# Kernel optimization log

Hardware: AMD Instinct MI355X
Metric: run time of the kernel (lower is better)

The kernel has to match this reference:

```python
import jax, jax.numpy as jnp
import numpy as np

B, S, D, H = 8, 1024, 1024, 16
DH = D // H  # 64

def setup_inputs() -> dict:
    key = jax.random.key(0)
    k1, k2, k3 = jax.random.split(key, 3)
    x = jax.random.normal(k1, (B, S, D), dtype=jnp.float32)
    mask = jnp.tril(jnp.ones((S, S), dtype=bool))[None, None]  # causal [1,1,S,S]
    W_qkv = jax.random.normal(k2, (D, 3 * D), dtype=jnp.float32) * 0.02
    W_out = jax.random.normal(k3, (D, D), dtype=jnp.float32) * 0.02
    return {"x": x, "mask": mask, "W_qkv": W_qkv, "W_out": W_out}

def reference(x, mask, W_qkv, W_out):
    qkv = jnp.einsum('bnd,de->bne', x, W_qkv)
    q, k, v = jnp.split(qkv, 3, axis=-1)
    # [b, h, n, dh]
    split_heads = lambda t: t.reshape(B, S, H, DH).transpose(0, 2, 1, 3)
    q, k, v = map(split_heads, (q, k, v))
    attn = jnp.einsum('bhnd,bhmd->bhnm', q, k) / jnp.sqrt(jnp.float32(DH))
    attn = jnp.where(mask, attn, 0.7 * jnp.finfo(attn.dtype).min)
    attn = jax.nn.softmax(attn.astype(jnp.float32), axis=-1).astype(x.dtype)
    out = jnp.einsum('bhnm,bhmd->bhnd', attn, v)
    out = out.transpose(0, 2, 1, 3).reshape(B, S, D)
    return jnp.einsum('bnd,de->bne', out, W_out)
```

## Files before the change

### kernel.cpp

```cpp
#include <hip/hip_runtime.h>
#include <stdint.h>

typedef __attribute__((ext_vector_type(8))) short short8;
typedef __attribute__((ext_vector_type(4))) float floatx4;

__device__ __forceinline__ unsigned short f2bf(float f) {
  union { float f; uint32_t u; } v; v.f = f;
  uint32_t u = v.u;
  return (unsigned short)((u + 0x7FFFu + ((u >> 16) & 1u)) >> 16);
}

__device__ __forceinline__ uint32_t fbits(float f) {
  union { float f; uint32_t u; } v; v.f = f; return v.u;
}
__device__ __forceinline__ uint32_t pkbf(float hi, float lo) {
  return __builtin_amdgcn_perm(fbits(hi), fbits(lo), 0x07060302u);
}

__device__ __forceinline__ void gl_lds16(const void* g, void* l) {
  __builtin_amdgcn_global_load_lds((__attribute__((address_space(1))) void*)g,
                                   (__attribute__((address_space(3))) void*)l,
                                   16, 0, 0);
}

__global__ __launch_bounds__(256) void prep_kernel(const float* __restrict__ x,
                                                   unsigned short* __restrict__ xb,
                                                   const float* __restrict__ Wqkv,
                                                   unsigned short* __restrict__ WqkvT,
                                                   const float* __restrict__ Wout,
                                                   unsigned short* __restrict__ WoutT) {
  __shared__ float tile[32][33];
  int id = blockIdx.x;
  if (id < 8192) {
    int i = id * 256 + threadIdx.x;
    float4 v = ((const float4*)x)[i];
    ushort4 o;
    o.x = f2bf(v.x); o.y = f2bf(v.y); o.z = f2bf(v.z); o.w = f2bf(v.w);
    ((ushort4*)xb)[i] = o;
    return;
  }
  id -= 8192;
  int bx = id & 127, r0 = (id >> 7) * 32;
  const int R = 1024;
  const float* in; unsigned short* out; int C;
  if (bx < 96) { in = Wqkv; out = WqkvT; C = 3072; }
  else         { in = Wout; out = WoutT; C = 1024; bx -= 96; }
  int c0 = bx * 32;
  int tx = threadIdx.x & 31;
  int ty = threadIdx.x >> 5;
  for (int i = ty; i < 32; i += 8)
    tile[i][tx] = in[(size_t)(r0 + i) * C + c0 + tx];
  __syncthreads();
  for (int i = ty; i < 32; i += 8)
    out[(size_t)(c0 + i) * R + r0 + tx] = f2bf(tile[tx][i]);
}

__global__ __launch_bounds__(256) void gemm_bt_kernel(const unsigned short* __restrict__ A,
                                                      const unsigned short* __restrict__ Bt,
                                                      int N, int mode,
                                                      unsigned short* __restrict__ qo,
                                                      unsigned short* __restrict__ ko,
                                                      unsigned short* __restrict__ vo,
                                                      float* __restrict__ fo) {
  const int Kd = 1024;
  __shared__ union {
    struct { unsigned short A[2][8192]; unsigned short B[2][8192]; } s;
    float cf[16384];
    unsigned short ch[32768];
  } sm;
  const int tid = threadIdx.x;
  const int w = tid >> 6, lane = tid & 63;
  const int quad = lane >> 4, l16 = lane & 15;
  const int l7 = l16 & 7;
  const int wm = w >> 1, wn = w & 1;
  const int m0 = blockIdx.y * 128, n0 = blockIdx.x * 128;
  const int tr = (mode == 0) && (n0 >= 2048);
  const int r8 = lane >> 3, ch = lane & 7;
  const int sw = (ch ^ r8) * 8;

  floatx4 acc[4][4];
#pragma unroll
  for (int i = 0; i < 4; ++i)
#pragma unroll
    for (int j = 0; j < 4; ++j)
      acc[i][j] = (floatx4){0.f, 0.f, 0.f, 0.f};

  auto stage = [&](int it, int buf) {
    const int k0 = it * 64;
#pragma unroll
    for (int i = 0; i < 4; ++i) {
      const int row = i * 32 + w * 8 + r8;
      gl_lds16(A + (size_t)(m0 + row) * Kd + k0 + sw, (char*)&sm.s.A[buf][0] + i * 4096 + w * 1024);
      gl_lds16(Bt + (size_t)(n0 + row) * Kd + k0 + sw, (char*)&sm.s.B[buf][0] + i * 4096 + w * 1024);
    }
  };

  stage(0, 0);
  __syncthreads();

  for (int it = 0; it < 16; ++it) {
    const int buf = it & 1;
    if (it < 15) stage(it + 1, buf ^ 1);
    const char* Ab = (const char*)&sm.s.A[buf][0];
    const char* Bb = (const char*)&sm.s.B[buf][0];
#pragma unroll
    for (int half = 0; half < 2; ++half) {
      short8 af[4], bf[4];
#pragma unroll
      for (int i = 0; i < 4; ++i)
        af[i] = *(const short8*)(Ab + (wm * 64 + i * 16 + l16) * 128 +
                                 (((half << 2) | quad) ^ l7) * 16);
#pragma unroll
      for (int j = 0; j < 4; ++j)
        bf[j] = *(const short8*)(Bb + (wn * 64 + j * 16 + l16) * 128 +
                                 (((half << 2) | quad) ^ l7) * 16);
      if (!tr) {
#pragma unroll
        for (int i = 0; i < 4; ++i)
#pragma unroll
          for (int j = 0; j < 4; ++j)
            acc[i][j] = __builtin_amdgcn_mfma_f32_16x16x32_bf16(af[i], bf[j], acc[i][j], 0, 0, 0);
      } else {
#pragma unroll
        for (int p = 0; p < 4; ++p)
#pragma unroll
          for (int q = 0; q < 4; ++q)
            acc[p][q] = __builtin_amdgcn_mfma_f32_16x16x32_bf16(bf[p], af[q], acc[p][q], 0, 0, 0);
      }
    }
    __syncthreads();
  }

  if (mode == 1) {
    float* Cs = sm.cf;
#pragma unroll
    for (int i = 0; i < 4; ++i)
#pragma unroll
      for (int j = 0; j < 4; ++j)
#pragma unroll
        for (int r = 0; r < 4; ++r) {
          int row = wm * 64 + i * 16 + quad * 4 + r;
          int col = wn * 64 + j * 16 + l16;
          Cs[row * 128 + (col ^ ((row & 7) << 2))] = acc[i][j][r];
        }
    __syncthreads();
#pragma unroll
    for (int c = 0; c < 16; ++c) {
      int idx = c * 256 + tid;
      int row = idx >> 5, fc = idx & 31;
      float4 v = *(const float4*)&sm.cf[row * 128 + ((fc ^ (row & 7)) << 2)];
      *(float4*)&fo[(size_t)(m0 + row) * N + n0 + fc * 4] = v;
    }
  } else {
    unsigned short* Cs = sm.ch;
    if (!tr) {
#pragma unroll
      for (int i = 0; i < 4; ++i)
#pragma unroll
        for (int j = 0; j < 4; ++j)
#pragma unroll
          for (int r = 0; r < 4; ++r) {
            int row = wm * 64 + i * 16 + quad * 4 + r;
            int col = wn * 64 + j * 16 + l16;
            Cs[row * 128 + (col ^ ((row & 7) << 3))] = f2bf(acc[i][j][r]);
          }
    } else {
#pragma unroll
      for (int p = 0; p < 4; ++p)
#pragma unroll
        for (int q = 0; q < 4; ++q)
#pragma unroll
          for (int r = 0; r < 4; ++r) {
            int row = wn * 64 + p * 16 + quad * 4 + r;
            int col = wm * 64 + q * 16 + l16;
            Cs[row * 128 + (col ^ ((row & 7) << 3))] = f2bf(acc[p][q][r]);
          }
    }
    __syncthreads();
    unsigned short* dst0 = (n0 < 1024) ? qo : ko;
#pragma unroll
    for (int c = 0; c < 8; ++c) {
      int idx = c * 256 + tid;
      int row = idx >> 4, lc = idx & 15;
      short8 v = *(const short8*)&sm.ch[row * 128 + ((lc ^ (row & 7)) << 3)];
      int col = lc * 8;
      if (!tr) {
        int m = m0 + row, n = n0 + col;
        int h = (n & 1023) >> 6, dh = n & 63;
        int bb = m >> 10, s = m & 1023;
        *(short8*)&dst0[(size_t)(bb * 16 + h) * 65536 + (size_t)s * 64 + dh] = v;
      } else {
        int n = n0 + row, m = m0 + col;
        int h = (n & 1023) >> 6, dh = n & 63;
        int bb = m >> 10, s0 = m & 1023;
        *(short8*)&vo[(size_t)(bb * 16 + h) * 65536 + (size_t)dh * 1024 + s0] = v;
      }
    }
  }
}

__global__ __launch_bounds__(512, 2) void gemm_qkv_kernel(const unsigned short* __restrict__ A,
                                                          const unsigned short* __restrict__ Bt,
                                                          unsigned short* __restrict__ qo,
                                                          unsigned short* __restrict__ ko,
                                                          unsigned short* __restrict__ vo) {
  __shared__ union {
    struct { unsigned short A[2][16384]; unsigned short B[2][8192]; } s;
    unsigned short ch[49152];
  } sm;
  const int tid = threadIdx.x;
  const int w = tid >> 6, lane = tid & 63;
  const int quad = lane >> 4, l16 = lane & 15, l7 = l16 & 7;
  const int wm = w >> 1, wn = w & 1;
  const int m0 = blockIdx.y * 256, n0 = blockIdx.x * 128;
  const bool tr = (n0 >= 2048);
  const int r8 = lane >> 3, ch8 = lane & 7;
  const int sw = (ch8 ^ r8) * 8;

  floatx4 acc[16];
#pragma unroll
  for (int i = 0; i < 16; ++i) acc[i] = (floatx4){0.f, 0.f, 0.f, 0.f};

  auto stageA = [&](int t, int buf) {
    const int k0 = t * 64;
#pragma unroll
    for (int i = 0; i < 4; ++i) {
      const int row = i * 64 + w * 8 + r8;
      gl_lds16(A + (size_t)(m0 + row) * 1024 + k0 + sw,
               (char*)&sm.s.A[buf][0] + (i * 64 + w * 8) * 128);
    }
  };
  auto stageB = [&](int t, int buf) {
    const int k0 = t * 64;
#pragma unroll
    for (int i = 0; i < 2; ++i) {
      const int row = i * 64 + w * 8 + r8;
      gl_lds16(Bt + (size_t)(n0 + row) * 1024 + k0 + sw,
               (char*)&sm.s.B[buf][0] + (i * 64 + w * 8) * 128);
    }
  };

  stageA(0, 0); stageB(0, 0);
  stageA(1, 1); stageB(1, 1);
  asm volatile("s_waitcnt vmcnt(6)" ::: "memory");
  __builtin_amdgcn_s_barrier();

  const int cK0 = (quad ^ l7) * 16;
  const int cK1 = ((4 | quad) ^ l7) * 16;
  const int arow = (wm * 64 + l16) * 128;
  const int brow = (wn * 64 + l16) * 128;

  short8 af[2][2];
  short8 bf[2][2][2];

#define MFMA8(MH, NH)                                                              \
  do {                                                                             \
    if (!tr) {                                                                     \
      _Pragma("unroll") for (int kk = 0; kk < 2; ++kk)                             \
      _Pragma("unroll") for (int m = 0; m < 2; ++m)                                \
      _Pragma("unroll") for (int n = 0; n < 2; ++n)                                \
        acc[((MH)*2 + m) * 4 + (NH)*2 + n] = __builtin_amdgcn_mfma_f32_16x16x32_bf16( \
            af[m][kk], bf[NH][n][kk], acc[((MH)*2 + m) * 4 + (NH)*2 + n], 0, 0, 0);   \
    } else {                                                                       \
      _Pragma("unroll") for (int kk = 0; kk < 2; ++kk)                             \
      _Pragma("unroll") for (int n = 0; n < 2; ++n)                                \
      _Pragma("unroll") for (int m = 0; m < 2; ++m)                                \
        acc[((NH)*2 + n) * 4 + (MH)*2 + m] = __builtin_amdgcn_mfma_f32_16x16x32_bf16( \
            bf[NH][n][kk], af[m][kk], acc[((NH)*2 + n) * 4 + (MH)*2 + m], 0, 0, 0);   \
    }                                                                              \
  } while (0)

  for (int t = 0; t < 16; ++t) {
    const int buf = t & 1;
    const char* Ab = (const char*)&sm.s.A[buf][0];
    const char* Bb = (const char*)&sm.s.B[buf][0];

#pragma unroll
    for (int m = 0; m < 2; ++m) {
      af[m][0] = *(const short8*)(Ab + arow + m * 2048 + cK0);
      af[m][1] = *(const short8*)(Ab + arow + m * 2048 + cK1);
    }
#pragma unroll
    for (int n = 0; n < 2; ++n) {
      bf[0][n][0] = *(const short8*)(Bb + brow + n * 2048 + cK0);
      bf[0][n][1] = *(const short8*)(Bb + brow + n * 2048 + cK1);
    }
    __builtin_amdgcn_s_barrier();
    asm volatile("s_waitcnt lgkmcnt(0)" ::: "memory");
    __builtin_amdgcn_s_setprio(1);
    MFMA8(0, 0);
    __builtin_amdgcn_s_setprio(0);
    __builtin_amdgcn_sched_barrier(0);
    __builtin_amdgcn_s_barrier();

#pragma unroll
    for (int n = 0; n < 2; ++n) {
      bf[1][n][0] = *(const short8*)(Bb + brow + (2 + n) * 2048 + cK0);
      bf[1][n][1] = *(const short8*)(Bb + brow + (2 + n) * 2048 + cK1);
    }
    __builtin_amdgcn_s_barrier();
    asm volatile("s_waitcnt lgkmcnt(0)" ::: "memory");
    __builtin_amdgcn_s_setprio(1);
    MFMA8(0, 1);
    __builtin_amdgcn_s_setprio(0);
    __builtin_amdgcn_sched_barrier(0);
    __builtin_amdgcn_s_barrier();

#pragma unroll
    for (int m = 0; m < 2; ++m) {
      af[m][0] = *(const short8*)(Ab + arow + (2 + m) * 2048 + cK0);
      af[m][1] = *(const short8*)(Ab + arow + (2 + m) * 2048 + cK1);
    }
    if (t < 14) stageB(t + 2, buf);
    __builtin_amdgcn_s_barrier();
    asm volatile("s_waitcnt lgkmcnt(0)" ::: "memory");
    __builtin_amdgcn_s_setprio(1);
    MFMA8(1, 1);
    __builtin_amdgcn_s_setprio(0);
    __builtin_amdgcn_sched_barrier(0);
    __builtin_amdgcn_s_barrier();

    if (t < 14) {
      stageA(t + 2, buf);
      asm volatile("s_waitcnt vmcnt(6)" ::: "memory");
    } else {
      asm volatile("s_waitcnt vmcnt(0)" ::: "memory");
    }
    __builtin_amdgcn_s_barrier();
    __builtin_amdgcn_s_setprio(1);
    MFMA8(1, 0);
    __builtin_amdgcn_s_setprio(0);
    __builtin_amdgcn_sched_barrier(0);
    __builtin_amdgcn_s_barrier();
  }
#undef MFMA8

  unsigned short* Cs = sm.ch;
  if (!tr) {
#pragma unroll
    for (int mf = 0; mf < 4; ++mf)
#pragma unroll
      for (int nf = 0; nf < 4; ++nf)
#pragma unroll
        for (int r = 0; r < 4; ++r) {
          int row = wm * 64 + mf * 16 + quad * 4 + r;
          int col = wn * 64 + nf * 16 + l16;
          Cs[row * 128 + (col ^ ((row & 7) << 3))] = f2bf(acc[mf * 4 + nf][r]);
        }
    __syncthreads();
    unsigned short* dst0 = (n0 < 1024) ? qo : ko;
#pragma unroll
    for (int c = 0; c < 8; ++c) {
      int idx = c * 512 + tid;
      int row = idx >> 4, lc = idx & 15;
      short8 v = *(const short8*)&Cs[row * 128 + ((lc ^ (row & 7)) << 3)];
      int m = m0 + row, n = n0 + lc * 8;
      int h = (n & 1023) >> 6, dh = n & 63;
      int bb = m >> 10, s = m & 1023;
      *(short8*)&dst0[(size_t)(bb * 16 + h) * 65536 + (size_t)s * 64 + dh] = v;
    }
  } else {
#pragma unroll
    for (int nf = 0; nf < 4; ++nf)
#pragma unroll
      for (int mf = 0; mf < 4; ++mf)
#pragma unroll
        for (int r = 0; r < 4; ++r) {
          int row = wn * 64 + nf * 16 + quad * 4 + r;
          int col = wm * 64 + mf * 16 + l16;
          Cs[row * 256 + (col ^ ((row & 7) << 3))] = f2bf(acc[nf * 4 + mf][r]);
        }
    __syncthreads();
#pragma unroll
    for (int c = 0; c < 8; ++c) {
      int idx = c * 512 + tid;
      int row = idx >> 5, lc = idx & 31;
      short8 v = *(const short8*)&Cs[row * 256 + ((lc ^ (row & 7)) << 3)];
      int n = n0 + row, m = m0 + lc * 8;
      int h = (n & 1023) >> 6, dh = n & 63;
      int bb = m >> 10, s = m & 1023;
      *(short8*)&vo[(size_t)(bb * 16 + h) * 65536 + (size_t)dh * 1024 + s] = v;
    }
  }
}

__global__ __launch_bounds__(256, 2) void attn_kernel(const unsigned short* __restrict__ Qb,
                                                      const unsigned short* __restrict__ Kb,
                                                      const unsigned short* __restrict__ VbT,
                                                      unsigned short* __restrict__ AOb) {
  __shared__ unsigned short Kt[2][4096];
  __shared__ unsigned short Vt[2][4096];
  const int tid = threadIdx.x;
  const int w = tid >> 6, lane = tid & 63;
  const int quad = lane >> 4, l16 = lane & 15;
  const int l7 = l16 & 7;
  const int id = blockIdx.x;
  const int by = id >> 2;
  const int p = id & 3;
  const int bb = by >> 4, hh = by & 15;
  const int qlo = p * 128 + w * 32;
  const int qhi = (7 - p) * 128 + w * 32;
  const unsigned short* Qp = Qb + (size_t)by * 65536;
  const unsigned short* Kp = Kb + (size_t)by * 65536;
  const unsigned short* Vp = VbT + (size_t)by * 65536;

  short8 bq[2][2][2];
#pragma unroll
  for (int g = 0; g < 2; ++g)
#pragma unroll
    for (int qt = 0; qt < 2; ++qt)
#pragma unroll
      for (int kh = 0; kh < 2; ++kh)
        bq[g][qt][kh] = *(const short8*)(Qp + (size_t)((g ? qhi : qlo) + qt * 16 + l16) * 64 +
                                         kh * 32 + quad * 8);

  floatx4 o[2][2][4];
  floatx4 ps[2][2];
#pragma unroll
  for (int g = 0; g < 2; ++g)
#pragma unroll
    for (int qt = 0; qt < 2; ++qt) {
      ps[g][qt] = (floatx4){0.f, 0.f, 0.f, 0.f};
#pragma unroll
      for (int dt = 0; dt < 4; ++dt) o[g][qt][dt] = (floatx4){0.f, 0.f, 0.f, 0.f};
    }

  short8 ones;
#pragma unroll
  for (int i = 0; i < 8; ++i) ones[i] = (short)0x3F80;

  const int T = 16 - 2 * p;
  const int r8 = lane >> 3, ch = lane & 7;
  const int sw8 = (ch ^ r8) * 8;

  auto stage = [&](int t, int buf) {
    const int n0 = t * 64;
#pragma unroll
    for (int i = 0; i < 2; ++i) {
      const int c = w * 2 + i;
      const int row = c * 8 + r8;
      gl_lds16(Kp + (size_t)(n0 + row) * 64 + sw8, (char*)&Kt[buf][0] + c * 1024);
      gl_lds16(Vp + (size_t)row * 1024 + n0 + sw8, (char*)&Vt[buf][0] + c * 1024);
    }
  };

  stage(0, 0);
  __syncthreads();

  for (int t = 0; t < T; ++t) {
    const int buf = t & 1;
    if (t + 1 < T) stage(t + 1, buf ^ 1);
    const int n0 = t * 64;
    const bool alo = (n0 <= qlo + 31), ahi = (n0 <= qhi + 31);
    if (alo | ahi) {
      const char* kbase = (const char*)&Kt[buf][0];
      const char* vbase = (const char*)&Vt[buf][0];
      short8 ak[4][2];
#pragma unroll
      for (int kt = 0; kt < 4; ++kt)
#pragma unroll
        for (int kh = 0; kh < 2; ++kh)
          ak[kt][kh] = *(const short8*)(kbase + (kt * 16 + l16) * 128 +
                                        (((kh << 2) | quad) ^ l7) * 16);
      union PaU { short8 v; uint32_t d[4]; };
      PaU pa[2][2][2];

      auto score = [&](int g, int qb) {
        const bool full = (n0 + 63 <= qb);
#pragma unroll
        for (int kt = 0; kt < 4; ++kt)
#pragma unroll
          for (int qt = 0; qt < 2; ++qt) {
            floatx4 s = (floatx4){0.f, 0.f, 0.f, 0.f};
            s = __builtin_amdgcn_mfma_f32_16x16x32_bf16(ak[kt][0], bq[g][qt][0], s, 0, 0, 0);
            s = __builtin_amdgcn_mfma_f32_16x16x32_bf16(ak[kt][1], bq[g][qt][1], s, 0, 0, 0);
            float f[4];
            if (full) {
#pragma unroll
              for (int r = 0; r < 4; ++r)
                f[r] = exp2f(fmaf(s[r], 0.18033688f, -11.5415603f));
            } else {
              const int query = qb + qt * 16 + l16;
#pragma unroll
              for (int r = 0; r < 4; ++r) {
                const int key = n0 + kt * 16 + quad * 4 + r;
                float e = exp2f(fmaf(s[r], 0.18033688f, -11.5415603f));
                f[r] = (key <= query) ? e : 0.0f;
              }
            }
            pa[g][qt][kt >> 1].d[(kt & 1) * 2 + 0] = pkbf(f[1], f[0]);
            pa[g][qt][kt >> 1].d[(kt & 1) * 2 + 1] = pkbf(f[3], f[2]);
          }
#pragma unroll
        for (int qt = 0; qt < 2; ++qt)
#pragma unroll
          for (int u = 0; u < 2; ++u)
            ps[g][qt] = __builtin_amdgcn_mfma_f32_16x16x32_bf16(pa[g][qt][u].v, ones, ps[g][qt], 0, 0, 0);
      };
      if (alo) score(0, qlo);
      if (ahi) score(1, qhi);

#pragma unroll
      for (int dt = 0; dt < 4; ++dt) {
        const int row128 = (dt * 16 + l16) * 128;
#pragma unroll
        for (int u = 0; u < 2; ++u) {
          union { short8 v8; ushort4 h[2]; } bv;
          bv.h[0] = *(const ushort4*)(vbase + row128 +
                                      (((u << 2) | (quad >> 1)) ^ l7) * 16 + (quad & 1) * 8);
          bv.h[1] = *(const ushort4*)(vbase + row128 +
                                      (((u << 2) | 2 | (quad >> 1)) ^ l7) * 16 + (quad & 1) * 8);
          if (alo) {
#pragma unroll
            for (int qt = 0; qt < 2; ++qt)
              o[0][qt][dt] = __builtin_amdgcn_mfma_f32_16x16x32_bf16(pa[0][qt][u].v, bv.v8, o[0][qt][dt], 0, 0, 0);
          }
          if (ahi) {
#pragma unroll
            for (int qt = 0; qt < 2; ++qt)
              o[1][qt][dt] = __builtin_amdgcn_mfma_f32_16x16x32_bf16(pa[1][qt][u].v, bv.v8, o[1][qt][dt], 0, 0, 0);
          }
        }
      }
    }
    __syncthreads();
  }

#pragma unroll
  for (int g = 0; g < 2; ++g) {
    const int qb = g ? qhi : qlo;
#pragma unroll
    for (int qt = 0; qt < 2; ++qt) {
      float inv[4];
#pragma unroll
      for (int r = 0; r < 4; ++r) inv[r] = 1.0f / ps[g][qt][r];
#pragma unroll
      for (int dt = 0; dt < 4; ++dt)
#pragma unroll
        for (int r = 0; r < 4; ++r) {
          int row = qb + qt * 16 + quad * 4 + r;
          AOb[(size_t)(bb * 1024 + row) * 1024 + hh * 64 + dt * 16 + l16] =
              f2bf(o[g][qt][dt][r] * inv[r]);
        }
    }
  }
}

extern "C" void kernel_launch(void* const* d_in, const int* in_sizes, int n_in,
                              void* d_out, int out_size, void* d_ws, size_t ws_size,
                              hipStream_t stream) {
  const float* x    = (const float*)d_in[0];
  const float* Wqkv = (const float*)d_in[2];
  const float* Wout = (const float*)d_in[3];
  float* out = (float*)d_out;

  unsigned short* xb    = (unsigned short*)d_ws;
  unsigned short* WqkvT = xb    + (size_t)8 * 1024 * 1024;
  unsigned short* WoutT = WqkvT + (size_t)3 * 1024 * 1024;
  unsigned short* Qb    = WoutT + (size_t)1024 * 1024;
  unsigned short* Kb    = Qb    + (size_t)8 * 1024 * 1024;
  unsigned short* VbT   = Kb    + (size_t)8 * 1024 * 1024;
  unsigned short* AOb   = VbT   + (size_t)8 * 1024 * 1024;

  prep_kernel<<<12288, 256, 0, stream>>>(x, xb, Wqkv, WqkvT, Wout, WoutT);
  gemm_qkv_kernel<<<dim3(24, 32), 512, 0, stream>>>(xb, WqkvT, Qb, Kb, VbT);
  attn_kernel<<<512, 256, 0, stream>>>(Qb, Kb, VbT, AOb);
  gemm_bt_kernel<<<dim3(8, 64), 256, 0, stream>>>(AOb, WoutT, 1024, 1, nullptr, nullptr, nullptr, out);
}
```

Measured before the change: 242.0 us.

## Restructure QKV GEMM main loop to prefetch LDS fragments across K-halves

Replaces the four-phase per-tile MFMA schedule with two 16-MFMA clusters split by K-half. Fragments for the next tile's first K-half are read from LDS while the current second K-half computes, so LDS reads overlap with MFMA work. The number of barriers per iteration drops from eight to two, and the A and B global-to-LDS stages are issued together. In exchange the kernel holds more fragment registers, and the partial lgkmcnt waits have to be exactly right for correctness.

After: 229.2 us. 5.3% less time.

```diff
diff --git a/kernel.cpp b/kernel.cpp
--- a/kernel.cpp
+++ b/kernel.cpp
@@ -240,100 +240,81 @@
     }
   };
 
+  const int cK0 = (quad ^ l7) * 16;
+  const int cK1 = ((4 | quad) ^ l7) * 16;
+  const int arow = (wm * 64 + l16) * 128;
+  const int brow = (wn * 64 + l16) * 128;
+
+  short8 af[4][2], bfr[4][2];
+
+  auto readF = [&](int buf2, int kk) {
+    const char* Ab2 = (const char*)&sm.s.A[buf2][0];
+    const char* Bb2 = (const char*)&sm.s.B[buf2][0];
+    const int cK = kk ? cK1 : cK0;
+#pragma unroll
+    for (int mf = 0; mf < 4; ++mf)
+      af[mf][kk] = *(const short8*)(Ab2 + arow + mf * 2048 + cK);
+#pragma unroll
+    for (int nf = 0; nf < 4; ++nf)
+      bfr[nf][kk] = *(const short8*)(Bb2 + brow + nf * 2048 + cK);
+  };
+
+#define CLUSTER(KK)                                                                 \
+  do {                                                                              \
+    if (!tr) {                                                                      \
+      _Pragma("unroll") for (int mf = 0; mf < 4; ++mf)                              \
+      _Pragma("unroll") for (int nf = 0; nf < 4; ++nf)                              \
+        acc[mf * 4 + nf] = __builtin_amdgcn_mfma_f32_16x16x32_bf16(                 \
+            af[mf][KK], bfr[nf][KK], acc[mf * 4 + nf], 0, 0, 0);                    \
+    } else {                                                                        \
+      _Pragma("unroll") for (int nf = 0; nf < 4; ++nf)                              \
+      _Pragma("unroll") for (int mf = 0; mf < 4; ++mf)                              \
+        acc[nf * 4 + mf] = __builtin_amdgcn_mfma_f32_16x16x32_bf16(                 \
+            bfr[nf][KK], af[mf][KK], acc[nf * 4 + mf], 0, 0, 0);                    \
+    }                                                                               \
+  } while (0)
+
   stageA(0, 0); stageB(0, 0);
   stageA(1, 1); stageB(1, 1);
   asm volatile("s_waitcnt vmcnt(6)" ::: "memory");
   __builtin_amdgcn_s_barrier();
-
-  const int cK0 = (quad ^ l7) * 16;
-  const int cK1 = ((4 | quad) ^ l7) * 16;
-  const int arow = (wm * 64 + l16) * 128;
-  const int brow = (wn * 64 + l16) * 128;
-
-  short8 af[2][2];
-  short8 bf[2][2][2];
-
-#define MFMA8(MH, NH)                                                              \
-  do {                                                                             \
-    if (!tr) {                                                                     \
-      _Pragma("unroll") for (int kk = 0; kk < 2; ++kk)                             \
-      _Pragma("unroll") for (int m = 0; m < 2; ++m)                                \
-      _Pragma("unroll") for (int n = 0; n < 2; ++n)                                \
-        acc[((MH)*2 + m) * 4 + (NH)*2 + n] = __builtin_amdgcn_mfma_f32_16x16x32_bf16( \
-            af[m][kk], bf[NH][n][kk], acc[((MH)*2 + m) * 4 + (NH)*2 + n], 0, 0, 0);   \
-    } else {                                                                       \
-      _Pragma("unroll") for (int kk = 0; kk < 2; ++kk)                             \
-      _Pragma("unroll") for (int n = 0; n < 2; ++n)                                \
-      _Pragma("unroll") for (int m = 0; m < 2; ++m)                                \
-        acc[((NH)*2 + n) * 4 + (MH)*2 + m] = __builtin_amdgcn_mfma_f32_16x16x32_bf16( \
-            bf[NH][n][kk], af[m][kk], acc[((NH)*2 + n) * 4 + (MH)*2 + m], 0, 0, 0);   \
-    }                                                                              \
-  } while (0)
+  readF(0, 0);
+  __builtin_amdgcn_sched_barrier(0);
+  readF(0, 1);
+  __builtin_amdgcn_sched_barrier(0);
 
   for (int t = 0; t < 16; ++t) {
     const int buf = t & 1;
-    const char* Ab = (const char*)&sm.s.A[buf][0];
-    const char* Bb = (const char*)&sm.s.B[buf][0];
-
-#pragma unroll
-    for (int m = 0; m < 2; ++m) {
-      af[m][0] = *(const short8*)(Ab + arow + m * 2048 + cK0);
-      af[m][1] = *(const short8*)(Ab + arow + m * 2048 + cK1);
-    }
-#pragma unroll
-    for (int n = 0; n < 2; ++n) {
-      bf[0][n][0] = *(const short8*)(Bb + brow + n * 2048 + cK0);
-      bf[0][n][1] = *(const short8*)(Bb + brow + n * 2048 + cK1);
-    }
-    __builtin_amdgcn_s_barrier();
-    asm volatile("s_waitcnt lgkmcnt(0)" ::: "memory");
+    asm volatile("s_waitcnt lgkmcnt(8)" ::: "memory");
+    __builtin_amdgcn_sched_barrier(0);
     __builtin_amdgcn_s_setprio(1);
-    MFMA8(0, 0);
+    CLUSTER(0);
     __builtin_amdgcn_s_setprio(0);
     __builtin_amdgcn_sched_barrier(0);
-    __builtin_amdgcn_s_barrier();
-
-#pragma unroll
-    for (int n = 0; n < 2; ++n) {
-      bf[1][n][0] = *(const short8*)(Bb + brow + (2 + n) * 2048 + cK0);
-      bf[1][n][1] = *(const short8*)(Bb + brow + (2 + n) * 2048 + cK1);
-    }
-    __builtin_amdgcn_s_barrier();
     asm volatile("s_waitcnt lgkmcnt(0)" ::: "memory");
-    __builtin_amdgcn_s_setprio(1);
-    MFMA8(0, 1);
-    __builtin_amdgcn_s_setprio(0);
     __builtin_amdgcn_sched_barrier(0);
     __builtin_amdgcn_s_barrier();
-
-#pragma unroll
-    for (int m = 0; m < 2; ++m) {
-      af[m][0] = *(const short8*)(Ab + arow + (2 + m) * 2048 + cK0);
-      af[m][1] = *(const short8*)(Ab + arow + (2 + m) * 2048 + cK1);
-    }
-    if (t < 14) stageB(t + 2, buf);
-    __builtin_amdgcn_s_barrier();
-    asm volatile("s_waitcnt lgkmcnt(0)" ::: "memory");
-    __builtin_amdgcn_s_setprio(1);
-    MFMA8(1, 1);
-    __builtin_amdgcn_s_setprio(0);
-    __builtin_amdgcn_sched_barrier(0);
-    __builtin_amdgcn_s_barrier();
-
     if (t < 14) {
-      stageA(t + 2, buf);
+      stageA(t + 2, buf); stageB(t + 2, buf);
       asm volatile("s_waitcnt vmcnt(6)" ::: "memory");
     } else {
       asm volatile("s_waitcnt vmcnt(0)" ::: "memory");
     }
     __builtin_amdgcn_s_barrier();
+    if (t < 15) {
+      readF(buf ^ 1, 0);
+      __builtin_amdgcn_sched_barrier(0);
+    }
     __builtin_amdgcn_s_setprio(1);
-    MFMA8(1, 0);
+    CLUSTER(1);
     __builtin_amdgcn_s_setprio(0);
     __builtin_amdgcn_sched_barrier(0);
-    __builtin_amdgcn_s_barrier();
-  }
-#undef MFMA8
+    if (t < 15) {
+      readF(buf ^ 1, 1);
+      __builtin_amdgcn_sched_barrier(0);
+    }
+  }
+#undef CLUSTER
 
   unsigned short* Cs = sm.ch;
   if (!tr) {
```
